# Kernel optimization log

Hardware: AMD Instinct MI355X
Metric: run time of the kernel (lower is better)

## Reference

```python
import jax, jax.numpy as jnp
import numpy as np

N = 100000
EPS_BN = 1e-5


def setup_inputs() -> dict:
    key = jax.random.key(0)
    ks = jax.random.split(key, 12)
    x = jax.random.normal(ks[0], (N, 128), dtype=jnp.float32)
    edge_index = jax.random.randint(ks[1], (2, 800000), 0, N, dtype=jnp.int64)
    # GCNConv layer params (PyG: lin weight [out,in], bias added after aggregation)
    s = 1.0 / np.sqrt(128.0)
    W1 = jax.random.uniform(ks[2], (128, 128), jnp.float32, -s, s)
    b1 = jnp.zeros((128,), jnp.float32)
    W2 = jax.random.uniform(ks[3], (128, 128), jnp.float32, -s, s)
    b2 = jnp.zeros((128,), jnp.float32)
    # BatchNorm affine params
    g1 = jnp.ones((128,), jnp.float32)
    be1 = jnp.zeros((128,), jnp.float32)
    g2 = jnp.ones((128,), jnp.float32)
    be2 = jnp.zeros((128,), jnp.float32)
    # PReLU single shared parameter (torch init = 0.25)
    a = jnp.asarray(0.25, jnp.float32)
    return {"x": x, "edge_index": edge_index, "W1": W1, "b1": b1, "g1": g1,
            "be1": be1, "W2": W2, "b2": b2, "g2": g2, "be2": be2, "a": a}


def _gcn_conv(x, src, dst, deg_inv_sqrt, W, b):
    # x' = D^-1/2 (A+I) D^-1/2 (x W^T) + b  (self loops already in src/dst)
    h = x @ W.T                                   # [N, out]
    norm = deg_inv_sqrt[src] * deg_inv_sqrt[dst]  # [E+N]
    msg = h[src] * norm[:, None]                  # gather + scale
    out = jax.ops.segment_sum(msg, dst, num_segments=N)  # scatter-add
    return out + b


def _batchnorm(x, g, be):
    # training-mode BatchNorm1d over nodes (biased variance)
    mean = jnp.mean(x, axis=0)
    var = jnp.mean(jnp.square(x - mean), axis=0)
    return (x - mean) * jax.lax.rsqrt(var + EPS_BN) * g + be


def _prelu(x, a):
    return jnp.where(x > 0, x, a * x)


def reference(x, edge_index, W1, b1, g1, be1, W2, b2, g2, be2, a):
    # add self loops
    loops = jnp.arange(N, dtype=edge_index.dtype)
    src = jnp.concatenate([edge_index[0], loops])
    dst = jnp.concatenate([edge_index[1], loops])
    # symmetric normalization from in-degree at destinations
    deg = jax.ops.segment_sum(jnp.ones_like(dst, dtype=x.dtype), dst, num_segments=N)
    deg_inv_sqrt = jnp.where(deg > 0, jax.lax.rsqrt(deg), 0.0)

    h = _gcn_conv(x, src, dst, deg_inv_sqrt, W1, b1)
    h = _prelu(_batchnorm(h, g1, be1), a)
    h = _gcn_conv(h, src, dst, deg_inv_sqrt, W2, b2)
    h = _prelu(_batchnorm(h, g2, be2), a)
    return h
```

## Files before the change

kernel.cpp:

```cpp
#include <hip/hip_runtime.h>
#include <cstddef>
#include <cstdint>


#define EPS_BN 1e-5f

typedef short short8 __attribute__((ext_vector_type(8)));
typedef float f32x4 __attribute__((ext_vector_type(4)));

static __device__ __forceinline__ unsigned short f2b(float f) {
    union { float f; uint32_t u; } v; v.f = f;
    uint32_t u = v.u;
    return (unsigned short)((u + 0x7FFFu + ((u >> 16) & 1u)) >> 16);
}
static __device__ __forceinline__ float b2f(unsigned short h) {
    union { uint32_t u; float f; } v; v.u = ((uint32_t)h) << 16;
    return v.f;
}
static __device__ __forceinline__ float b2f_s(short h) { return b2f((unsigned short)h); }

__global__ __launch_bounds__(256) void k_prep(const float* __restrict__ W1, const float* __restrict__ W2,
                                              unsigned short* __restrict__ Wz1, unsigned short* __restrict__ Wz2,
                                              const int* __restrict__ dst, int* __restrict__ cnt,
                                              int* __restrict__ rank, int E) {
    int bid = blockIdx.x, tid = threadIdx.x;
    if (bid < 128) {
        int gi = bid * 256 + tid;
        const float* W = (gi < 16384) ? W1 : W2;
        unsigned short* Wz = (gi < 16384) ? Wz1 : Wz2;
        int idx = gi & 16383;
        int o = idx >> 7, k = idx & 127;
        int ct = o >> 4, nn = o & 15, ks = k >> 5, q = (k >> 3) & 3, j = k & 7;
        Wz[(ct * 4 + ks) * 512 + (q * 16 + nn) * 8 + j] = f2b(W[idx]);
    } else {
        int e = (bid - 128) * 256 + tid;
        if (e < E) rank[e] = atomicAdd(&cnt[dst[e]], 1);
    }
}

__global__ __launch_bounds__(256) void k_scanA(const int* __restrict__ cnt, int* __restrict__ partial, int n) {
    __shared__ int sd[256];
    int tid = threadIdx.x;
    int base = blockIdx.x * 1024 + tid * 4;
    int s = 0;
#pragma unroll
    for (int j = 0; j < 4; j++) { int idx = base + j; if (idx < n) s += cnt[idx]; }
    sd[tid] = s; __syncthreads();
    for (int off = 128; off > 0; off >>= 1) {
        if (tid < off) sd[tid] += sd[tid + off];
        __syncthreads();
    }
    if (tid == 0) partial[blockIdx.x] = sd[0];
}

__global__ __launch_bounds__(256) void k_scanC(const int* __restrict__ cnt, const int* __restrict__ partial,
                                               int* __restrict__ rowptr, float* __restrict__ dis, int n, int nb) {
    __shared__ int sp[256];
    __shared__ int sd[256];
    int tid = threadIdx.x;
    sp[tid] = (tid < nb) ? partial[tid] : 0;
    int base = blockIdx.x * 1024 + tid * 4;
    int v[4]; int s = 0;
#pragma unroll
    for (int j = 0; j < 4; j++) { int idx = base + j; v[j] = (idx < n) ? cnt[idx] : 0; s += v[j]; }
    sd[tid] = s;
    __syncthreads();
    for (int off = 1; off < 256; off <<= 1) {
        int a = (tid >= off) ? sp[tid - off] : 0;
        int b = (tid >= off) ? sd[tid - off] : 0;
        __syncthreads();
        sp[tid] += a; sd[tid] += b;
        __syncthreads();
    }
    int gbase = (blockIdx.x == 0) ? 0 : sp[blockIdx.x - 1];
    int excl = gbase + ((tid == 0) ? 0 : sd[tid - 1]);
#pragma unroll
    for (int j = 0; j < 4; j++) {
        int idx = base + j;
        if (idx < n) {
            rowptr[idx] = excl;
            dis[idx] = rsqrtf((float)(v[j] + 1));
        }
        excl += v[j];
    }
}

__global__ __launch_bounds__(256) void k_fill_gemm1(const float* __restrict__ X,
                                                    const unsigned short* __restrict__ Wz,
                                                    unsigned short* __restrict__ Yb, int n,
                                                    const int* __restrict__ src, const int* __restrict__ dst,
                                                    const int* __restrict__ rowptr, const int* __restrict__ rank,
                                                    int* __restrict__ colw, int E, int gGemm) {
    __shared__ unsigned short lds[16384];
    int tid = threadIdx.x;
    if ((int)blockIdx.x >= gGemm) {
        int e = (blockIdx.x - gGemm) * 256 + tid;
        if (e < E) {
            int d = dst[e];
            colw[rowptr[d] + rank[e]] = src[e];
        }
        return;
    }
    const short8* wsrc = (const short8*)Wz;
    short8* ldst = (short8*)lds;
#pragma unroll
    for (int i = 0; i < 8; i++) ldst[tid + 256 * i] = wsrc[tid + 256 * i];
    __syncthreads();

    int wave = tid >> 6, lane = tid & 63;
    int mrow = lane & 15, quad = lane >> 4;
    int r0w = blockIdx.x * 256 + wave * 64;

    for (int s = 0; s < 4; ++s) {
        int r0 = r0w + s * 16;
        int arow = r0 + mrow; if (arow > n - 1) arow = n - 1;
        const float* xr = X + (size_t)arow * 128;

        f32x4 acc[8];
#pragma unroll
        for (int ct = 0; ct < 8; ct++) acc[ct] = (f32x4){0.f, 0.f, 0.f, 0.f};

#pragma unroll
        for (int ks = 0; ks < 4; ks++) {
            int kb = ks * 32 + quad * 8;
            float4 x0 = *reinterpret_cast<const float4*>(xr + kb);
            float4 x1 = *reinterpret_cast<const float4*>(xr + kb + 4);
            short8 a;
            a[0] = (short)f2b(x0.x); a[1] = (short)f2b(x0.y); a[2] = (short)f2b(x0.z); a[3] = (short)f2b(x0.w);
            a[4] = (short)f2b(x1.x); a[5] = (short)f2b(x1.y); a[6] = (short)f2b(x1.z); a[7] = (short)f2b(x1.w);
#pragma unroll
            for (int ct = 0; ct < 8; ct++) {
                short8 b = *(const short8*)(lds + (ct * 4 + ks) * 512 + lane * 8);
                acc[ct] = __builtin_amdgcn_mfma_f32_16x16x32_bf16(a, b, acc[ct], 0, 0, 0);
            }
        }
#pragma unroll
        for (int i = 0; i < 4; i++) {
            int row = r0 + quad * 4 + i;
            if (row < n) {
#pragma unroll
                for (int ct = 0; ct < 8; ct++)
                    Yb[(size_t)row * 128 + ct * 16 + mrow] = f2b(acc[ct][i]);
            }
        }
    }
}

__global__ __launch_bounds__(256) void k_gemm2(const unsigned short* __restrict__ Ab,
                                               const unsigned short* __restrict__ Wz,
                                               const float* __restrict__ acc1,
                                               const float* __restrict__ g1, const float* __restrict__ be1,
                                               const float* __restrict__ ap,
                                               unsigned short* __restrict__ Yb, float invN, int n) {
    __shared__ unsigned short lds[16384];
    __shared__ float scl[128];
    __shared__ float shl[128];
    int tid = threadIdx.x;
    if (tid < 128) {
        float mean = acc1[tid] * invN;
        float var = acc1[128 + tid] * invN - mean * mean;
        float rstd = rsqrtf(var + EPS_BN);
        float scale = g1[tid] * rstd;
        scl[tid] = scale;
        shl[tid] = fmaf(-mean, scale, be1[tid]);
    }
    const short8* wsrc = (const short8*)Wz;
    short8* ldst = (short8*)lds;
#pragma unroll
    for (int i = 0; i < 8; i++) ldst[tid + 256 * i] = wsrc[tid + 256 * i];
    __syncthreads();

    float alpha = ap[0];
    int wave = tid >> 6, lane = tid & 63;
    int mrow = lane & 15, quad = lane >> 4;
    int r0w = blockIdx.x * 256 + wave * 64;

    for (int s = 0; s < 4; ++s) {
        int r0 = r0w + s * 16;
        int arow = r0 + mrow; if (arow > n - 1) arow = n - 1;
        const unsigned short* ar = Ab + (size_t)arow * 128;

        f32x4 acc[8];
#pragma unroll
        for (int ct = 0; ct < 8; ct++) acc[ct] = (f32x4){0.f, 0.f, 0.f, 0.f};

#pragma unroll
        for (int ks = 0; ks < 4; ks++) {
            int kb = ks * 32 + quad * 8;
            short8 raw = *(const short8*)(ar + kb);
            float4 s0 = *reinterpret_cast<const float4*>(scl + kb);
            float4 s1 = *reinterpret_cast<const float4*>(scl + kb + 4);
            float4 t0 = *reinterpret_cast<const float4*>(shl + kb);
            float4 t1 = *reinterpret_cast<const float4*>(shl + kb + 4);
            float ss[8] = {s0.x, s0.y, s0.z, s0.w, s1.x, s1.y, s1.z, s1.w};
            float tt[8] = {t0.x, t0.y, t0.z, t0.w, t1.x, t1.y, t1.z, t1.w};
            short8 a;
#pragma unroll
            for (int j = 0; j < 8; j++) {
                float x = fmaf(b2f_s(raw[j]), ss[j], tt[j]);
                x = x > 0.f ? x : alpha * x;
                a[j] = (short)f2b(x);
            }
#pragma unroll
            for (int ct = 0; ct < 8; ct++) {
                short8 b = *(const short8*)(lds + (ct * 4 + ks) * 512 + lane * 8);
                acc[ct] = __builtin_amdgcn_mfma_f32_16x16x32_bf16(a, b, acc[ct], 0, 0, 0);
            }
        }
#pragma unroll
        for (int i = 0; i < 4; i++) {
            int row = r0 + quad * 4 + i;
            if (row < n) {
#pragma unroll
                for (int ct = 0; ct < 8; ct++)
                    Yb[(size_t)row * 128 + ct * 16 + mrow] = f2b(acc[ct][i]);
            }
        }
    }
}

__global__ __launch_bounds__(256) void k_aggst(const unsigned short* __restrict__ Hb,
                                               const int* __restrict__ rowptr, const int* __restrict__ cnt,
                                               const int* __restrict__ colw, const float* __restrict__ dis,
                                               const float* __restrict__ bias,
                                               unsigned short* __restrict__ outb,
                                               float* __restrict__ part, int n) {
    __shared__ float ls[16][128];
    __shared__ float lq[16][128];
    int tid = threadIdx.x;
    int lane = tid & 15, slot = tid >> 4;
    int node = blockIdx.x * 16 + slot;
    bool act = node < n;
    int nodec = act ? node : (n - 1);
    int lo = lane * 8;
    float dn = dis[nodec];
    short8 hv = *(const short8*)(Hb + (size_t)nodec * 128 + lo);
    float acc[8];
#pragma unroll
    for (int j = 0; j < 8; j++) acc[j] = dn * b2f_s(hv[j]);
    int num = act ? cnt[nodec] : 0;
    int beg = rowptr[nodec];
    const int* cw = colw + beg;
    int e = 0;
    for (; e + 4 <= num; e += 4) {
        int s0 = cw[e], s1 = cw[e + 1], s2 = cw[e + 2], s3 = cw[e + 3];
        float w0 = dis[s0], w1 = dis[s1], w2 = dis[s2], w3 = dis[s3];
        short8 n0 = *(const short8*)(Hb + (size_t)s0 * 128 + lo);
        short8 n1 = *(const short8*)(Hb + (size_t)s1 * 128 + lo);
        short8 n2 = *(const short8*)(Hb + (size_t)s2 * 128 + lo);
        short8 n3 = *(const short8*)(Hb + (size_t)s3 * 128 + lo);
#pragma unroll
        for (int j = 0; j < 8; j++) {
            acc[j] = fmaf(w0, b2f_s(n0[j]), acc[j]);
            acc[j] = fmaf(w1, b2f_s(n1[j]), acc[j]);
            acc[j] = fmaf(w2, b2f_s(n2[j]), acc[j]);
            acc[j] = fmaf(w3, b2f_s(n3[j]), acc[j]);
        }
    }
    for (; e < num; ++e) {
        int s = cw[e];
        float w = dis[s];
        short8 nb = *(const short8*)(Hb + (size_t)s * 128 + lo);
#pragma unroll
        for (int j = 0; j < 8; j++) acc[j] = fmaf(w, b2f_s(nb[j]), acc[j]);
    }
    const float4 bv0 = reinterpret_cast<const float4*>(bias)[lane * 2 + 0];
    const float4 bv1 = reinterpret_cast<const float4*>(bias)[lane * 2 + 1];
    float bb[8] = {bv0.x, bv0.y, bv0.z, bv0.w, bv1.x, bv1.y, bv1.z, bv1.w};
    short8 ov;
    float fv[8];
#pragma unroll
    for (int j = 0; j < 8; j++) {
        float y = fmaf(dn, acc[j], bb[j]);
        unsigned short h = f2b(y);
        ov[j] = (short)h;
        fv[j] = act ? b2f(h) : 0.f;
    }
    if (act) *(short8*)(outb + (size_t)node * 128 + lo) = ov;
#pragma unroll
    for (int j = 0; j < 8; j++) {
        ls[slot][lane * 8 + j] = fv[j];
        lq[slot][lane * 8 + j] = fv[j] * fv[j];
    }
    __syncthreads();
    for (int off = 8; off > 0; off >>= 1) {
        if (slot < off) {
#pragma unroll
            for (int j = 0; j < 8; j++) {
                ls[slot][lane * 8 + j] += ls[slot + off][lane * 8 + j];
                lq[slot][lane * 8 + j] += lq[slot + off][lane * 8 + j];
            }
        }
        __syncthreads();
    }
    if (tid < 128) part[(size_t)blockIdx.x * 256 + tid] = ls[0][tid];
    else           part[(size_t)blockIdx.x * 256 + tid] = lq[0][tid - 128];
}

__global__ __launch_bounds__(256) void k_bnred(const float* __restrict__ part, float* __restrict__ acc, int nb) {
    int tid = threadIdx.x;
    float s = 0.f;
    for (int b = blockIdx.x; b < nb; b += gridDim.x) s += part[(size_t)b * 256 + tid];
    atomicAdd(&acc[tid], s);
}

__global__ __launch_bounds__(256) void k_bnact_f(const unsigned short* __restrict__ X, float* __restrict__ Y,
                                                 const float* __restrict__ acc2,
                                                 const float* __restrict__ g2, const float* __restrict__ be2,
                                                 const float* __restrict__ ap, float invN, int n8) {
    __shared__ float scl[128];
    __shared__ float shl[128];
    int tid = threadIdx.x;
    if (tid < 128) {
        float mean = acc2[tid] * invN;
        float var = acc2[128 + tid] * invN - mean * mean;
        float rstd = rsqrtf(var + EPS_BN);
        float scale = g2[tid] * rstd;
        scl[tid] = scale;
        shl[tid] = fmaf(-mean, scale, be2[tid]);
    }
    __syncthreads();
    int i = blockIdx.x * 256 + tid;
    if (i >= n8) return;
    float a = ap[0];
    int g = i & 15;
    const float4 s0 = reinterpret_cast<const float4*>(scl)[g * 2 + 0];
    const float4 s1 = reinterpret_cast<const float4*>(scl)[g * 2 + 1];
    const float4 t0 = reinterpret_cast<const float4*>(shl)[g * 2 + 0];
    const float4 t1 = reinterpret_cast<const float4*>(shl)[g * 2 + 1];
    float ss[8] = {s0.x, s0.y, s0.z, s0.w, s1.x, s1.y, s1.z, s1.w};
    float tt[8] = {t0.x, t0.y, t0.z, t0.w, t1.x, t1.y, t1.z, t1.w};
    short8 v = reinterpret_cast<const short8*>(X)[i];
    float out[8];
#pragma unroll
    for (int j = 0; j < 8; j++) {
        float x = fmaf(b2f_s(v[j]), ss[j], tt[j]);
        out[j] = x > 0.f ? x : a * x;
    }
    float4 o0 = {out[0], out[1], out[2], out[3]};
    float4 o1 = {out[4], out[5], out[6], out[7]};
    reinterpret_cast<float4*>(Y)[i * 2 + 0] = o0;
    reinterpret_cast<float4*>(Y)[i * 2 + 1] = o1;
}

extern "C" void kernel_launch(void* const* d_in, const int* in_sizes, int n_in,
                              void* d_out, int out_size, void* d_ws, size_t ws_size,
                              hipStream_t stream) {
    (void)n_in; (void)out_size; (void)ws_size;
    const float* x   = (const float*)d_in[0];
    const int*   ei  = (const int*)d_in[1];
    const float* W1  = (const float*)d_in[2];
    const float* b1  = (const float*)d_in[3];
    const float* g1  = (const float*)d_in[4];
    const float* be1 = (const float*)d_in[5];
    const float* W2  = (const float*)d_in[6];
    const float* b2  = (const float*)d_in[7];
    const float* g2  = (const float*)d_in[8];
    const float* be2 = (const float*)d_in[9];
    const float* ap  = (const float*)d_in[10];
    float* out = (float*)d_out;

    const int N = in_sizes[0] / 128;
    const int E = in_sizes[1] / 2;
    const int* srcIdx = ei;
    const int* dstIdx = ei + E;

    const int NB = (N + 1023) / 1024;
    const int gE = (E + 255) / 256;
    const int n8 = N * 16;
    const int gGemm = (N + 255) / 256;
    const int gAgg  = (N + 15) / 16;

    char* w = (char*)d_ws;
    size_t off = 0;
    auto alloc = [&](size_t bytes) { char* p = w + off; off += (bytes + 255) & ~(size_t)255; return p; };
    int*   cnt     = (int*)  alloc((size_t)N * 4);
    float* acc1    = (float*)alloc(1024);
    float* acc2    = (float*)alloc(1024);
    size_t zero_bytes = off;
    int*   rowptr  = (int*)  alloc((size_t)N * 4);
    int*   rank    = (int*)  alloc((size_t)E * 4);
    int*   colw    = (int*)  alloc((size_t)E * 4);
    float* dis     = (float*)alloc((size_t)N * 4);
    int*   partial = (int*)  alloc(4096);
    float* part    = (float*)alloc((size_t)gAgg * 256 * 4);
    unsigned short* Wz1 = (unsigned short*)alloc(16384 * 2);
    unsigned short* Wz2 = (unsigned short*)alloc(16384 * 2);
    unsigned short* bufH = (unsigned short*)alloc((size_t)N * 128 * 2);
    unsigned short* bufA = (unsigned short*)alloc((size_t)N * 128 * 2);

    const float invN = 1.0f / (float)N;

    hipMemsetAsync(cnt, 0, zero_bytes, stream);

    k_prep<<<128 + gE, 256, 0, stream>>>(W1, W2, Wz1, Wz2, dstIdx, cnt, rank, E);

    k_scanA<<<NB, 256, 0, stream>>>(cnt, partial, N);
    k_scanC<<<NB, 256, 0, stream>>>(cnt, partial, rowptr, dis, N, NB);

    k_fill_gemm1<<<gGemm + gE, 256, 0, stream>>>(x, Wz1, bufH, N,
                                                 srcIdx, dstIdx, rowptr, rank, colw, E, gGemm);
    k_aggst<<<gAgg, 256, 0, stream>>>(bufH, rowptr, cnt, colw, dis, b1, bufA, part, N);
    k_bnred<<<64, 256, 0, stream>>>(part, acc1, gAgg);

    k_gemm2<<<gGemm, 256, 0, stream>>>(bufA, Wz2, acc1, g1, be1, ap, bufH, invN, N);
    k_aggst<<<gAgg, 256, 0, stream>>>(bufH, rowptr, cnt, colw, dis, b2, bufA, part, N);
    k_bnred<<<64, 256, 0, stream>>>(part, acc2, gAgg);
    k_bnact_f<<<(n8 + 255) / 256, 256, 0, stream>>>(bufA, out, acc2, g2, be2, ap, invN, n8);
}
```

Measured before the change: 353.7 us.

## Shrink GEMM blocks to 64 rows and use wave shuffles for BN partial sums

The two GEMM kernels now handle 64 rows per block, one 16-row tile per wave, instead of looping over four tiles, and the grid grows four times to match. This is meant to raise parallelism and occupancy, at the cost of loading the weight matrix into LDS four times as often. The aggregation kernel's BatchNorm partial-sum reduction now uses cross-lane xor shuffles inside each wave. It then does a single 4-way LDS sum, replacing the multi-step LDS tree with a barrier after each step, which cuts LDS traffic and barriers.

```diff
diff --git a/kernel.cpp b/kernel.cpp
--- a/kernel.cpp
+++ b/kernel.cpp
@@ -108,40 +108,36 @@
     __syncthreads();
 
     int wave = tid >> 6, lane = tid & 63;
+    int r0 = blockIdx.x * 64 + wave * 16;
     int mrow = lane & 15, quad = lane >> 4;
-    int r0w = blockIdx.x * 256 + wave * 64;
-
-    for (int s = 0; s < 4; ++s) {
-        int r0 = r0w + s * 16;
-        int arow = r0 + mrow; if (arow > n - 1) arow = n - 1;
-        const float* xr = X + (size_t)arow * 128;
-
-        f32x4 acc[8];
-#pragma unroll
-        for (int ct = 0; ct < 8; ct++) acc[ct] = (f32x4){0.f, 0.f, 0.f, 0.f};
-
-#pragma unroll
-        for (int ks = 0; ks < 4; ks++) {
-            int kb = ks * 32 + quad * 8;
-            float4 x0 = *reinterpret_cast<const float4*>(xr + kb);
-            float4 x1 = *reinterpret_cast<const float4*>(xr + kb + 4);
-            short8 a;
-            a[0] = (short)f2b(x0.x); a[1] = (short)f2b(x0.y); a[2] = (short)f2b(x0.z); a[3] = (short)f2b(x0.w);
-            a[4] = (short)f2b(x1.x); a[5] = (short)f2b(x1.y); a[6] = (short)f2b(x1.z); a[7] = (short)f2b(x1.w);
-#pragma unroll
-            for (int ct = 0; ct < 8; ct++) {
-                short8 b = *(const short8*)(lds + (ct * 4 + ks) * 512 + lane * 8);
-                acc[ct] = __builtin_amdgcn_mfma_f32_16x16x32_bf16(a, b, acc[ct], 0, 0, 0);
-            }
-        }
-#pragma unroll
-        for (int i = 0; i < 4; i++) {
-            int row = r0 + quad * 4 + i;
-            if (row < n) {
-#pragma unroll
-                for (int ct = 0; ct < 8; ct++)
-                    Yb[(size_t)row * 128 + ct * 16 + mrow] = f2b(acc[ct][i]);
-            }
+    int arow = r0 + mrow; if (arow > n - 1) arow = n - 1;
+    const float* xr = X + (size_t)arow * 128;
+
+    f32x4 acc[8];
+#pragma unroll
+    for (int ct = 0; ct < 8; ct++) acc[ct] = (f32x4){0.f, 0.f, 0.f, 0.f};
+
+#pragma unroll
+    for (int ks = 0; ks < 4; ks++) {
+        int kb = ks * 32 + quad * 8;
+        float4 x0 = *reinterpret_cast<const float4*>(xr + kb);
+        float4 x1 = *reinterpret_cast<const float4*>(xr + kb + 4);
+        short8 a;
+        a[0] = (short)f2b(x0.x); a[1] = (short)f2b(x0.y); a[2] = (short)f2b(x0.z); a[3] = (short)f2b(x0.w);
+        a[4] = (short)f2b(x1.x); a[5] = (short)f2b(x1.y); a[6] = (short)f2b(x1.z); a[7] = (short)f2b(x1.w);
+#pragma unroll
+        for (int ct = 0; ct < 8; ct++) {
+            short8 b = *(const short8*)(lds + (ct * 4 + ks) * 512 + lane * 8);
+            acc[ct] = __builtin_amdgcn_mfma_f32_16x16x32_bf16(a, b, acc[ct], 0, 0, 0);
+        }
+    }
+#pragma unroll
+    for (int i = 0; i < 4; i++) {
+        int row = r0 + quad * 4 + i;
+        if (row < n) {
+#pragma unroll
+            for (int ct = 0; ct < 8; ct++)
+                Yb[(size_t)row * 128 + ct * 16 + mrow] = f2b(acc[ct][i]);
         }
     }
 }
@@ -172,49 +168,45 @@
 
     float alpha = ap[0];
     int wave = tid >> 6, lane = tid & 63;
+    int r0 = blockIdx.x * 64 + wave * 16;
     int mrow = lane & 15, quad = lane >> 4;
-    int r0w = blockIdx.x * 256 + wave * 64;
-
-    for (int s = 0; s < 4; ++s) {
-        int r0 = r0w + s * 16;
-        int arow = r0 + mrow; if (arow > n - 1) arow = n - 1;
-        const unsigned short* ar = Ab + (size_t)arow * 128;
-
-        f32x4 acc[8];
-#pragma unroll
-        for (int ct = 0; ct < 8; ct++) acc[ct] = (f32x4){0.f, 0.f, 0.f, 0.f};
-
-#pragma unroll
-        for (int ks = 0; ks < 4; ks++) {
-            int kb = ks * 32 + quad * 8;
-            short8 raw = *(const short8*)(ar + kb);
-            float4 s0 = *reinterpret_cast<const float4*>(scl + kb);
-            float4 s1 = *reinterpret_cast<const float4*>(scl + kb + 4);
-            float4 t0 = *reinterpret_cast<const float4*>(shl + kb);
-            float4 t1 = *reinterpret_cast<const float4*>(shl + kb + 4);
-            float ss[8] = {s0.x, s0.y, s0.z, s0.w, s1.x, s1.y, s1.z, s1.w};
-            float tt[8] = {t0.x, t0.y, t0.z, t0.w, t1.x, t1.y, t1.z, t1.w};
-            short8 a;
-#pragma unroll
-            for (int j = 0; j < 8; j++) {
-                float x = fmaf(b2f_s(raw[j]), ss[j], tt[j]);
-                x = x > 0.f ? x : alpha * x;
-                a[j] = (short)f2b(x);
-            }
-#pragma unroll
-            for (int ct = 0; ct < 8; ct++) {
-                short8 b = *(const short8*)(lds + (ct * 4 + ks) * 512 + lane * 8);
-                acc[ct] = __builtin_amdgcn_mfma_f32_16x16x32_bf16(a, b, acc[ct], 0, 0, 0);
-            }
-        }
-#pragma unroll
-        for (int i = 0; i < 4; i++) {
-            int row = r0 + quad * 4 + i;
-            if (row < n) {
-#pragma unroll
-                for (int ct = 0; ct < 8; ct++)
-                    Yb[(size_t)row * 128 + ct * 16 + mrow] = f2b(acc[ct][i]);
-            }
+    int arow = r0 + mrow; if (arow > n - 1) arow = n - 1;
+    const unsigned short* ar = Ab + (size_t)arow * 128;
+
+    f32x4 acc[8];
+#pragma unroll
+    for (int ct = 0; ct < 8; ct++) acc[ct] = (f32x4){0.f, 0.f, 0.f, 0.f};
+
+#pragma unroll
+    for (int ks = 0; ks < 4; ks++) {
+        int kb = ks * 32 + quad * 8;
+        short8 raw = *(const short8*)(ar + kb);
+        float4 s0 = *reinterpret_cast<const float4*>(scl + kb);
+        float4 s1 = *reinterpret_cast<const float4*>(scl + kb + 4);
+        float4 t0 = *reinterpret_cast<const float4*>(shl + kb);
+        float4 t1 = *reinterpret_cast<const float4*>(shl + kb + 4);
+        float ss[8] = {s0.x, s0.y, s0.z, s0.w, s1.x, s1.y, s1.z, s1.w};
+        float tt[8] = {t0.x, t0.y, t0.z, t0.w, t1.x, t1.y, t1.z, t1.w};
+        short8 a;
+#pragma unroll
+        for (int j = 0; j < 8; j++) {
+            float x = fmaf(b2f_s(raw[j]), ss[j], tt[j]);
+            x = x > 0.f ? x : alpha * x;
+            a[j] = (short)f2b(x);
+        }
+#pragma unroll
+        for (int ct = 0; ct < 8; ct++) {
+            short8 b = *(const short8*)(lds + (ct * 4 + ks) * 512 + lane * 8);
+            acc[ct] = __builtin_amdgcn_mfma_f32_16x16x32_bf16(a, b, acc[ct], 0, 0, 0);
+        }
+    }
+#pragma unroll
+    for (int i = 0; i < 4; i++) {
+        int row = r0 + quad * 4 + i;
+        if (row < n) {
+#pragma unroll
+            for (int ct = 0; ct < 8; ct++)
+                Yb[(size_t)row * 128 + ct * 16 + mrow] = f2b(acc[ct][i]);
         }
     }
 }
@@ -225,8 +217,8 @@
                                                const float* __restrict__ bias,
                                                unsigned short* __restrict__ outb,
                                                float* __restrict__ part, int n) {
-    __shared__ float ls[16][128];
-    __shared__ float lq[16][128];
+    __shared__ float ls[4][128];
+    __shared__ float lq[4][128];
     int tid = threadIdx.x;
     int lane = tid & 15, slot = tid >> 4;
     int node = blockIdx.x * 16 + slot;
@@ -268,33 +260,41 @@
     const float4 bv1 = reinterpret_cast<const float4*>(bias)[lane * 2 + 1];
     float bb[8] = {bv0.x, bv0.y, bv0.z, bv0.w, bv1.x, bv1.y, bv1.z, bv1.w};
     short8 ov;
-    float fv[8];
+    float s8[8], q8[8];
 #pragma unroll
     for (int j = 0; j < 8; j++) {
         float y = fmaf(dn, acc[j], bb[j]);
         unsigned short h = f2b(y);
         ov[j] = (short)h;
-        fv[j] = act ? b2f(h) : 0.f;
+        float fv = act ? b2f(h) : 0.f;
+        s8[j] = fv;
+        q8[j] = fv * fv;
     }
     if (act) *(short8*)(outb + (size_t)node * 128 + lo) = ov;
 #pragma unroll
     for (int j = 0; j < 8; j++) {
-        ls[slot][lane * 8 + j] = fv[j];
-        lq[slot][lane * 8 + j] = fv[j] * fv[j];
+        s8[j] += __shfl_xor(s8[j], 16, 64);
+        q8[j] += __shfl_xor(q8[j], 16, 64);
+        s8[j] += __shfl_xor(s8[j], 32, 64);
+        q8[j] += __shfl_xor(q8[j], 32, 64);
+    }
+    int wave = tid >> 6;
+    if ((tid & 63) < 16) {
+#pragma unroll
+        for (int j = 0; j < 8; j++) {
+            ls[wave][lane * 8 + j] = s8[j];
+            lq[wave][lane * 8 + j] = q8[j];
+        }
     }
     __syncthreads();
-    for (int off = 8; off > 0; off >>= 1) {
-        if (slot < off) {
-#pragma unroll
-            for (int j = 0; j < 8; j++) {
-                ls[slot][lane * 8 + j] += ls[slot + off][lane * 8 + j];
-                lq[slot][lane * 8 + j] += lq[slot + off][lane * 8 + j];
-            }
-        }
-        __syncthreads();
-    }
-    if (tid < 128) part[(size_t)blockIdx.x * 256 + tid] = ls[0][tid];
-    else           part[(size_t)blockIdx.x * 256 + tid] = lq[0][tid - 128];
+    if (tid < 128) {
+        float r = ls[0][tid] + ls[1][tid] + ls[2][tid] + ls[3][tid];
+        part[(size_t)blockIdx.x * 256 + tid] = r;
+    } else {
+        int f = tid - 128;
+        float r = lq[0][f] + lq[1][f] + lq[2][f] + lq[3][f];
+        part[(size_t)blockIdx.x * 256 + 128 + f] = r;
+    }
 }
 
 __global__ __launch_bounds__(256) void k_bnred(const float* __restrict__ part, float* __restrict__ acc, int nb) {
@@ -368,7 +368,7 @@
     const int NB = (N + 1023) / 1024;
     const int gE = (E + 255) / 256;
     const int n8 = N * 16;
-    const int gGemm = (N + 255) / 256;
+    const int gGemm = (N + 63) / 64;
     const int gAgg  = (N + 15) / 16;
 
     char* w = (char*)d_ws;
```

Result: faster. 342.2 us (-3.3%).
